# Performance work log

Hardware: AMD Instinct MI355X
Metric: run time of the kernel (lower is better)

## Reference

```python
import jax, jax.numpy as jnp
import numpy as np

N = 50000      # nodes
E = 800000     # edges (avg degree 16)
D = 128        # in_dim
H = 128        # hidden_dim
C = 10         # num_classes
G = 128        # graphs in batch
NUM_LAYERS = 3


def setup_inputs() -> dict:
    key = jax.random.key(0)
    ks = jax.random.split(key, 32)
    inp = {
        'features': jax.random.normal(ks[0], (N, D), dtype=jnp.float32),
        'src': jax.random.randint(ks[1], (E,), 0, N, dtype=jnp.int32),
        'dst': jax.random.randint(ks[2], (E,), 0, N, dtype=jnp.int32),
        'graph_ids': jnp.sort(jax.random.randint(ks[3], (N,), 0, G, dtype=jnp.int32)),
        'eps': jnp.zeros((NUM_LAYERS,), dtype=jnp.float32),  # learn_eps=True, init 0
    }
    # GIN MLPs: layer i has linear1 [in,H], linear2 [H,H] (stored as [in,out])
    ki = 4
    for i in range(NUM_LAYERS):
        din = D if i == 0 else H
        inp[f'w1_{i}'] = jax.random.normal(ks[ki], (din, H), dtype=jnp.float32) * (1.0 / np.sqrt(din)); ki += 1
        inp[f'b1_{i}'] = jnp.zeros((H,), dtype=jnp.float32)
        inp[f'w2_{i}'] = jax.random.normal(ks[ki], (H, H), dtype=jnp.float32) * (1.0 / np.sqrt(H)); ki += 1
        inp[f'b2_{i}'] = jnp.zeros((H,), dtype=jnp.float32)
    inp['wc1'] = jax.random.normal(ks[ki], (H, H), dtype=jnp.float32) * (1.0 / np.sqrt(H)); ki += 1
    inp['bc1'] = jnp.zeros((H,), dtype=jnp.float32)
    inp['wc2'] = jax.random.normal(ks[ki], (H, C), dtype=jnp.float32) * (1.0 / np.sqrt(H)); ki += 1
    inp['bc2'] = jnp.zeros((C,), dtype=jnp.float32)
    return inp


def _mlp(x, w1, b1, w2, b2):
    return jax.nn.relu(x @ w1 + b1) @ w2 + b2


def reference(features, src, dst, graph_ids, eps,
              w1_0, b1_0, w2_0, b2_0,
              w1_1, b1_1, w2_1, b2_1,
              w1_2, b1_2, w2_2, b2_2,
              wc1, bc1, wc2, bc2):
    mlps = [(w1_0, b1_0, w2_0, b2_0), (w1_1, b1_1, w2_1, b2_1), (w1_2, b1_2, w2_2, b2_2)]
    h = features
    for i, (w1, b1, w2, b2) in enumerate(mlps):
        # GINConv: aggregate sum of in-neighbor features (gather src, segment-sum into dst)
        agg = jax.ops.segment_sum(h[src], dst, num_segments=N)
        h = (1.0 + eps[i]) * h + agg
        h = _mlp(h, w1, b1, w2, b2)
        h = jax.nn.relu(h)
    # SumPooling: nodes -> graphs
    hg = jax.ops.segment_sum(h, graph_ids, num_segments=G)  # [G, H]
    out = jax.nn.relu(hg @ wc1 + bc1) @ wc2 + bc2            # [G, C]
    return out
```

## Files before the change

### kernel.cpp

```cpp
#include <hip/hip_runtime.h>

#define NN 50000
#define EE 800000
#define HH 128
#define CC 10
#define GG 128
#define NBK 782
#define NCH 98
#define CHUNK 8192

typedef __attribute__((ext_vector_type(8))) short short8;
typedef __attribute__((ext_vector_type(4))) float f32x4;

__device__ __forceinline__ ushort f2b(float f) {
    union { float f; uint u; } x; x.f = f;
    uint u = x.u;
    uint r = (u + 0x7fffu + ((u >> 16) & 1u)) >> 16;
    return (ushort)r;
}
__device__ __forceinline__ float lo2f(uint v) {
    union { uint u; float f; } x; x.u = v << 16; return x.f;
}
__device__ __forceinline__ float hi2f(uint v) {
    union { uint u; float f; } x; x.u = v & 0xffff0000u; return x.f;
}


__global__ __launch_bounds__(256) void prep_kernel(const float* __restrict__ features,
                                                   const float* w0, const float* w1,
                                                   const float* w2, const float* w3,
                                                   const float* w4, const float* w5,
                                                   const int* __restrict__ dst,
                                                   ushort* __restrict__ hb0,
                                                   ushort* __restrict__ wt,
                                                   int* __restrict__ hist) {
    __shared__ int hc[NBK];
    const int b = blockIdx.x, t = threadIdx.x;
    if (b < 6250) {
        int idx = b * 256 + t;
        float4 v = *(const float4*)(features + (size_t)idx * 4);
        ushort4 o;
        o.x = f2b(v.x); o.y = f2b(v.y); o.z = f2b(v.z); o.w = f2b(v.w);
        *(ushort4*)(hb0 + (size_t)idx * 4) = o;
    } else if (b < 6634) {
        int idx = (b - 6250) * 256 + t;
        int mi = idx >> 14, rest = idx & 16383;
        int n = rest >> 7, k = rest & 127;
        const float* src;
        switch (mi) {
            case 0: src = w0; break; case 1: src = w1; break;
            case 2: src = w2; break; case 3: src = w3; break;
            case 4: src = w4; break; default: src = w5; break;
        }
        wt[mi * 16384 + n * 128 + k] = f2b(src[k * 128 + n]);
    } else {
        const int c = b - 6634;
        for (int k = t; k < NBK; k += 256) hc[k] = 0;
        __syncthreads();
        for (int j = 0; j < 32; ++j) {
            int e = c * CHUNK + j * 256 + t;
            if (e < EE) atomicAdd(&hc[dst[e] >> 6], 1);
        }
        __syncthreads();
        for (int k = t; k < NBK; k += 256) hist[k * NCH + c] = hc[k];
    }
}

__global__ __launch_bounds__(128) void bscan_kernel(const int* __restrict__ hist,
                                                    int* __restrict__ rel,
                                                    int* __restrict__ btot) {
    __shared__ int s[128];
    const int b = blockIdx.x, t = threadIdx.x;
    int v = (t < NCH) ? hist[b * NCH + t] : 0;
    s[t] = v;
    __syncthreads();
    for (int off = 1; off < 128; off <<= 1) {
        int tt = (t >= off) ? s[t - off] : 0;
        __syncthreads();
        s[t] += tt;
        __syncthreads();
    }
    if (t < NCH) rel[b * NCH + t] = s[t] - v;
    if (t == 127) btot[b] = s[127];
}

__global__ __launch_bounds__(1024) void tscan_kernel(const int* __restrict__ btot,
                                                     int* __restrict__ bucketptr,
                                                     int* __restrict__ rowptr) {
    __shared__ int s[1024];
    const int t = threadIdx.x;
    int v = (t < NBK) ? btot[t] : 0;
    s[t] = v;
    __syncthreads();
    for (int off = 1; off < 1024; off <<= 1) {
        int tt = (t >= off) ? s[t - off] : 0;
        __syncthreads();
        s[t] += tt;
        __syncthreads();
    }
    if (t < NBK) bucketptr[t] = s[t] - v;
    if (t == 0) { bucketptr[NBK] = EE; rowptr[NN] = EE; }
}

__global__ __launch_bounds__(256) void scatter_kernel(const int* __restrict__ src,
                                                      const int* __restrict__ dst,
                                                      const int* __restrict__ rel,
                                                      const int* __restrict__ bucketptr,
                                                      int* __restrict__ epk) {
    __shared__ int cur[NBK];
    const int c = blockIdx.x, t = threadIdx.x;
    for (int k = t; k < NBK; k += 256) cur[k] = bucketptr[k] + rel[k * NCH + c];
    __syncthreads();
    for (int j = 0; j < 32; ++j) {
        int e = c * CHUNK + j * 256 + t;
        if (e < EE) {
            int d = dst[e];
            int bk = d >> 6;
            int pos = atomicAdd(&cur[bk], 1);
            epk[pos] = ((d & 63) << 16) | src[e];
        }
    }
}

__global__ __launch_bounds__(256) void bsort_kernel(const int* __restrict__ epk,
                                                    const int* __restrict__ bucketptr,
                                                    ushort* __restrict__ eidx,
                                                    int* __restrict__ rowptr) {
    __shared__ int cnt[64];
    __shared__ int cur[64];
    const int b = blockIdx.x, t = threadIdx.x;
    const int base = bucketptr[b], end = bucketptr[b + 1];
    if (t < 64) cnt[t] = 0;
    __syncthreads();
    for (int i = base + t; i < end; i += 256)
        atomicAdd(&cnt[(epk[i] >> 16) & 63], 1);
    __syncthreads();
    if (t < 64) {
        int v = cnt[t];
        int incl = v;
#pragma unroll
        for (int off = 1; off < 64; off <<= 1) {
            int u = __shfl_up(incl, off);
            if (t >= off) incl += u;
        }
        int excl = incl - v;
        cur[t] = excl;
        int node = b * 64 + t;
        if (node < NN) rowptr[node] = base + excl;
    }
    __syncthreads();
    for (int i = base + t; i < end; i += 256) {
        int p = epk[i];
        int dl = (p >> 16) & 63;
        int pos = atomicAdd(&cur[dl], 1);
        eidx[base + pos] = (ushort)(p & 0xffff);
    }
}


__global__ __launch_bounds__(256) void aggregate_kernel(const ushort* __restrict__ h,
                                                        const int* __restrict__ rowptr,
                                                        const ushort* __restrict__ eidx,
                                                        const float* __restrict__ epsp,
                                                        int layer,
                                                        ushort* __restrict__ xb) {
    const int node = blockIdx.x * 8 + (threadIdx.x >> 5);
    if (node >= NN) return;
    const int li = threadIdx.x & 31;
    const int beg = rowptr[node], end = rowptr[node + 1];
    float c0 = 0.f, c1 = 0.f, c2 = 0.f, c3 = 0.f;
    int i = beg;
    for (; i + 8 <= end; i += 8) {
        int s[8];
        uint2 v[8];
#pragma unroll
        for (int k = 0; k < 8; ++k) s[k] = eidx[i + k];
#pragma unroll
        for (int k = 0; k < 8; ++k)
            v[k] = *(const uint2*)(h + (size_t)s[k] * HH + li * 4);
#pragma unroll
        for (int k = 0; k < 8; ++k) {
            c0 += lo2f(v[k].x); c1 += hi2f(v[k].x);
            c2 += lo2f(v[k].y); c3 += hi2f(v[k].y);
        }
    }
    for (; i < end; ++i) {
        int s = eidx[i];
        uint2 v = *(const uint2*)(h + (size_t)s * HH + li * 4);
        c0 += lo2f(v.x); c1 += hi2f(v.x);
        c2 += lo2f(v.y); c3 += hi2f(v.y);
    }
    uint2 hv = *(const uint2*)(h + (size_t)node * HH + li * 4);
    const float e = 1.0f + epsp[layer];
    ushort4 o;
    o.x = f2b(e * lo2f(hv.x) + c0);
    o.y = f2b(e * hi2f(hv.x) + c1);
    o.z = f2b(e * lo2f(hv.y) + c2);
    o.w = f2b(e * hi2f(hv.y) + c3);
    *(ushort4*)(xb + (size_t)node * HH + li * 4) = o;
}


template <bool LAST>
__global__ __launch_bounds__(256) void fused_mlp(const ushort* __restrict__ xb,
                                                 const ushort* __restrict__ wt1,
                                                 const ushort* __restrict__ wt2,
                                                 const float* __restrict__ b1,
                                                 const float* __restrict__ b2,
                                                 const int* __restrict__ gid,
                                                 float* __restrict__ hg,
                                                 ushort* __restrict__ out, int nrows) {
    __shared__ __align__(16) ushort xs[64][136];
    __shared__ __align__(16) ushort hs[64][136];
    const int tid = threadIdx.x;
    const int lane = tid & 63, w = tid >> 6;
    const int row0 = blockIdx.x * 64;
    const int l15 = lane & 15, lhi = lane >> 4;

    short8 a1[2][4], a2[2][4];
#pragma unroll
    for (int fa = 0; fa < 2; ++fa)
#pragma unroll
        for (int kt = 0; kt < 4; ++kt) {
            int n = w * 32 + fa * 16 + l15;
            int k = kt * 32 + lhi * 8;
            a1[fa][kt] = *(const short8*)(wt1 + n * HH + k);
            a2[fa][kt] = *(const short8*)(wt2 + n * HH + k);
        }

#pragma unroll
    for (int it = 0; it < 4; ++it) {
        int idx = it * 256 + tid;
        int r = idx >> 4, kq = idx & 15;
        int row = row0 + r;
        uint4 xv = make_uint4(0u, 0u, 0u, 0u);
        if (row < nrows) xv = *(const uint4*)(xb + (size_t)row * HH + kq * 8);
        *(uint4*)&xs[r][kq * 8] = xv;
    }
    __syncthreads();

    f32x4 acc[2][4];
#pragma unroll
    for (int fa = 0; fa < 2; ++fa)
#pragma unroll
        for (int fb = 0; fb < 4; ++fb) acc[fa][fb] = (f32x4)(0.f);
#pragma unroll
    for (int kt = 0; kt < 4; ++kt) {
        short8 bfr[4];
#pragma unroll
        for (int fb = 0; fb < 4; ++fb)
            bfr[fb] = *(const short8*)&xs[fb * 16 + l15][kt * 32 + lhi * 8];
#pragma unroll
        for (int fa = 0; fa < 2; ++fa)
#pragma unroll
            for (int fb = 0; fb < 4; ++fb)
                acc[fa][fb] = __builtin_amdgcn_mfma_f32_16x16x32_bf16(a1[fa][kt], bfr[fb],
                                                                     acc[fa][fb], 0, 0, 0);
    }

#pragma unroll
    for (int fa = 0; fa < 2; ++fa) {
        int nb = w * 32 + fa * 16 + lhi * 4;
        float4 bv = *(const float4*)(b1 + nb);
#pragma unroll
        for (int fb = 0; fb < 4; ++fb) {
            ushort4 o;
            o.x = f2b(fmaxf(acc[fa][fb][0] + bv.x, 0.f));
            o.y = f2b(fmaxf(acc[fa][fb][1] + bv.y, 0.f));
            o.z = f2b(fmaxf(acc[fa][fb][2] + bv.z, 0.f));
            o.w = f2b(fmaxf(acc[fa][fb][3] + bv.w, 0.f));
            *(ushort4*)&hs[fb * 16 + l15][nb] = o;
        }
    }
    __syncthreads();

#pragma unroll
    for (int fa = 0; fa < 2; ++fa)
#pragma unroll
        for (int fb = 0; fb < 4; ++fb) acc[fa][fb] = (f32x4)(0.f);
#pragma unroll
    for (int kt = 0; kt < 4; ++kt) {
        short8 bfr[4];
#pragma unroll
        for (int fb = 0; fb < 4; ++fb)
            bfr[fb] = *(const short8*)&hs[fb * 16 + l15][kt * 32 + lhi * 8];
#pragma unroll
        for (int fa = 0; fa < 2; ++fa)
#pragma unroll
            for (int fb = 0; fb < 4; ++fb)
                acc[fa][fb] = __builtin_amdgcn_mfma_f32_16x16x32_bf16(a2[fa][kt], bfr[fb],
                                                                     acc[fa][fb], 0, 0, 0);
    }

#pragma unroll
    for (int fa = 0; fa < 2; ++fa) {
        int nb = w * 32 + fa * 16 + lhi * 4;
        float4 bv = *(const float4*)(b2 + nb);
#pragma unroll
        for (int fb = 0; fb < 4; ++fb) {
            int m = row0 + fb * 16 + l15;
            ushort4 o;
            o.x = f2b(fmaxf(acc[fa][fb][0] + bv.x, 0.f));
            o.y = f2b(fmaxf(acc[fa][fb][1] + bv.y, 0.f));
            o.z = f2b(fmaxf(acc[fa][fb][2] + bv.z, 0.f));
            o.w = f2b(fmaxf(acc[fa][fb][3] + bv.w, 0.f));
            if (LAST) {
                *(ushort4*)&xs[fb * 16 + l15][nb] = o;
            } else if (m < nrows) {
                *(ushort4*)(out + (size_t)m * HH + nb) = o;
            }
        }
    }

    if (LAST) {
        __syncthreads();
        int j = tid & 63;
        int rg = tid >> 6;
        float ax = 0.f, ay = 0.f;
        int gcur = -1;
#pragma unroll
        for (int ii = 0; ii < 16; ++ii) {
            int r = rg + ii * 4;
            int n = row0 + r;
            if (n >= nrows) break;
            int g = gid[n];
            if (g != gcur) {
                if (gcur >= 0) {
                    atomicAdd(&hg[gcur * HH + 2 * j], ax);
                    atomicAdd(&hg[gcur * HH + 2 * j + 1], ay);
                }
                gcur = g; ax = 0.f; ay = 0.f;
            }
            uint v = *(const uint*)&xs[r][2 * j];
            ax += lo2f(v); ay += hi2f(v);
        }
        if (gcur >= 0) {
            atomicAdd(&hg[gcur * HH + 2 * j], ax);
            atomicAdd(&hg[gcur * HH + 2 * j + 1], ay);
        }
    }
}


__global__ __launch_bounds__(128) void classify_kernel(const float* __restrict__ hg,
                                                       const float* __restrict__ wc1,
                                                       const float* __restrict__ bc1,
                                                       const float* __restrict__ wc2,
                                                       const float* __restrict__ bc2,
                                                       float* __restrict__ out) {
    __shared__ float xrow[HH];
    __shared__ float trow[HH];
    int g = blockIdx.x, j = threadIdx.x;
    xrow[j] = hg[g * HH + j];
    __syncthreads();
    float s = bc1[j];
#pragma unroll 8
    for (int k = 0; k < HH; ++k) s += xrow[k] * wc1[k * HH + j];
    trow[j] = fmaxf(s, 0.f);
    __syncthreads();
    if (j < CC) {
        float o = bc2[j];
#pragma unroll 8
        for (int k = 0; k < HH; ++k) o += trow[k] * wc2[k * CC + j];
        out[g * CC + j] = o;
    }
}

extern "C" void kernel_launch(void* const* d_in, const int* in_sizes, int n_in,
                              void* d_out, int out_size, void* d_ws, size_t ws_size,
                              hipStream_t stream) {
    const float* features = (const float*)d_in[0];
    const int* src = (const int*)d_in[1];
    const int* dst = (const int*)d_in[2];
    const int* gid = (const int*)d_in[3];
    const float* eps = (const float*)d_in[4];
    const float* w1[3] = {(const float*)d_in[5], (const float*)d_in[9], (const float*)d_in[13]};
    const float* b1[3] = {(const float*)d_in[6], (const float*)d_in[10], (const float*)d_in[14]};
    const float* w2[3] = {(const float*)d_in[7], (const float*)d_in[11], (const float*)d_in[15]};
    const float* b2[3] = {(const float*)d_in[8], (const float*)d_in[12], (const float*)d_in[16]};
    const float* wc1 = (const float*)d_in[17];
    const float* bc1 = (const float*)d_in[18];
    const float* wc2 = (const float*)d_in[19];
    const float* bc2 = (const float*)d_in[20];
    float* outp = (float*)d_out;

    char* ws = (char*)d_ws;
    size_t off = 0;
    auto alloc = [&](size_t bytes) {
        void* p = ws + off;
        off += (bytes + 255) & ~(size_t)255;
        return p;
    };
    int* hist = (int*)alloc((size_t)NBK * NCH * sizeof(int));
    int* rel = (int*)alloc((size_t)NBK * NCH * sizeof(int));
    int* btot = (int*)alloc(NBK * sizeof(int));
    int* bucketptr = (int*)alloc((NBK + 1) * sizeof(int));
    int* epk = (int*)alloc(EE * sizeof(int));
    ushort* eidx = (ushort*)alloc(EE * sizeof(ushort));
    int* rowptr = (int*)alloc((NN + 1) * sizeof(int));
    ushort* hb0 = (ushort*)alloc((size_t)NN * HH * 2);
    ushort* hbuf = (ushort*)alloc((size_t)NN * HH * 2);
    ushort* xb = (ushort*)alloc((size_t)NN * HH * 2);
    ushort* wtb = (ushort*)alloc(6 * 16384 * 2);
    float* hg = (float*)alloc(GG * HH * sizeof(float));

    prep_kernel<<<6732, 256, 0, stream>>>(features, w1[0], w2[0], w1[1], w2[1], w1[2], w2[2],
                                          dst, hb0, wtb, hist);
    bscan_kernel<<<NBK, 128, 0, stream>>>(hist, rel, btot);
    tscan_kernel<<<1, 1024, 0, stream>>>(btot, bucketptr, rowptr);
    scatter_kernel<<<NCH, 256, 0, stream>>>(src, dst, rel, bucketptr, epk);
    bsort_kernel<<<NBK, 256, 0, stream>>>(epk, bucketptr, eidx, rowptr);

    hipMemsetAsync(hg, 0, GG * HH * sizeof(float), stream);

    const int GB = (NN + 63) / 64;
    const int AB = (NN + 7) / 8;

    aggregate_kernel<<<AB, 256, 0, stream>>>(hb0, rowptr, eidx, eps, 0, xb);
    fused_mlp<false><<<GB, 256, 0, stream>>>(xb, wtb + 0 * 16384, wtb + 1 * 16384,
                                             b1[0], b2[0], gid, hg, hbuf, NN);
    aggregate_kernel<<<AB, 256, 0, stream>>>(hbuf, rowptr, eidx, eps, 1, xb);
    fused_mlp<false><<<GB, 256, 0, stream>>>(xb, wtb + 2 * 16384, wtb + 3 * 16384,
                                             b1[1], b2[1], gid, hg, hbuf, NN);
    aggregate_kernel<<<AB, 256, 0, stream>>>(hbuf, rowptr, eidx, eps, 2, xb);
    fused_mlp<true><<<GB, 256, 0, stream>>>(xb, wtb + 4 * 16384, wtb + 5 * 16384,
                                            b1[2], b2[2], gid, hg, nullptr, NN);

    classify_kernel<<<GG, 128, 0, stream>>>(hg, wc1, bc1, wc2, bc2, outp);
}
```

Measured before the change: 230.2 us.

## Process two row tiles per MLP block with prefetch, fold memset, batch aggregate tail

The fused MLP now handles 128 rows per block as two 64-row tiles. The second tile's global loads are issued before the first tile's compute and written to shared memory afterwards, so the load latency overlaps with MFMA work and the weight-fragment loads are amortized over twice as many rows. The zeroing of hg moves into extra blocks of the prep kernel, which removes the separate memset launch. The aggregate kernel's remainder loop becomes one batched 8-wide gather with clamped indices and predicated accumulation, exposing more memory-level parallelism at the cost of redundant loads. Halving the number of MLP blocks and doubling shared memory per block can reduce occupancy.

```diff
diff --git a/kernel.cpp b/kernel.cpp
--- a/kernel.cpp
+++ b/kernel.cpp
@@ -33,7 +33,8 @@
                                                    const int* __restrict__ dst,
                                                    ushort* __restrict__ hb0,
                                                    ushort* __restrict__ wt,
-                                                   int* __restrict__ hist) {
+                                                   int* __restrict__ hist,
+                                                   float* __restrict__ hg) {
     __shared__ int hc[NBK];
     const int b = blockIdx.x, t = threadIdx.x;
     if (b < 6250) {
@@ -53,7 +54,7 @@
             case 4: src = w4; break; default: src = w5; break;
         }
         wt[mi * 16384 + n * 128 + k] = f2b(src[k * 128 + n]);
-    } else {
+    } else if (b < 6732) {
         const int c = b - 6634;
         for (int k = t; k < NBK; k += 256) hc[k] = 0;
         __syncthreads();
@@ -63,6 +64,9 @@
         }
         __syncthreads();
         for (int k = t; k < NBK; k += 256) hist[k * NCH + c] = hc[k];
+    } else {
+        int idx = (b - 6732) * 256 + t;
+        hg[idx] = 0.f;
     }
 }
 
@@ -184,11 +188,24 @@
             c2 += lo2f(v[k].y); c3 += hi2f(v[k].y);
         }
     }
-    for (; i < end; ++i) {
-        int s = eidx[i];
-        uint2 v = *(const uint2*)(h + (size_t)s * HH + li * 4);
-        c0 += lo2f(v.x); c1 += hi2f(v.x);
-        c2 += lo2f(v.y); c3 += hi2f(v.y);
+    if (i < end) {
+        int s[8];
+        uint2 v[8];
+#pragma unroll
+        for (int k = 0; k < 8; ++k) {
+            int idx = i + k;
+            s[k] = eidx[idx < end ? idx : end - 1];
+        }
+#pragma unroll
+        for (int k = 0; k < 8; ++k)
+            v[k] = *(const uint2*)(h + (size_t)s[k] * HH + li * 4);
+#pragma unroll
+        for (int k = 0; k < 8; ++k) {
+            if (i + k < end) {
+                c0 += lo2f(v[k].x); c1 += hi2f(v[k].x);
+                c2 += lo2f(v[k].y); c3 += hi2f(v[k].y);
+            }
+        }
     }
     uint2 hv = *(const uint2*)(h + (size_t)node * HH + li * 4);
     const float e = 1.0f + epsp[layer];
@@ -210,12 +227,22 @@
                                                  const int* __restrict__ gid,
                                                  float* __restrict__ hg,
                                                  ushort* __restrict__ out, int nrows) {
-    __shared__ __align__(16) ushort xs[64][136];
+    __shared__ __align__(16) ushort xs[2][64][136];
     __shared__ __align__(16) ushort hs[64][136];
     const int tid = threadIdx.x;
     const int lane = tid & 63, w = tid >> 6;
-    const int row0 = blockIdx.x * 64;
+    const int row0 = blockIdx.x * 128;
     const int l15 = lane & 15, lhi = lane >> 4;
+    const int sr = tid >> 4, skq = tid & 15;
+
+    uint4 st[4];
+#pragma unroll
+    for (int it = 0; it < 4; ++it) {
+        int r = it * 16 + sr;
+        int row = row0 + r;
+        st[it] = make_uint4(0u, 0u, 0u, 0u);
+        if (row < nrows) st[it] = *(const uint4*)(xb + (size_t)row * HH + skq * 8);
+    }
 
     short8 a1[2][4], a2[2][4];
 #pragma unroll
@@ -229,114 +256,119 @@
         }
 
 #pragma unroll
+    for (int it = 0; it < 4; ++it) *(uint4*)&xs[0][it * 16 + sr][skq * 8] = st[it];
+    __syncthreads();
+
+#pragma unroll
     for (int it = 0; it < 4; ++it) {
-        int idx = it * 256 + tid;
-        int r = idx >> 4, kq = idx & 15;
-        int row = row0 + r;
-        uint4 xv = make_uint4(0u, 0u, 0u, 0u);
-        if (row < nrows) xv = *(const uint4*)(xb + (size_t)row * HH + kq * 8);
-        *(uint4*)&xs[r][kq * 8] = xv;
-    }
-    __syncthreads();
+        int r = it * 16 + sr;
+        int row = row0 + 64 + r;
+        st[it] = make_uint4(0u, 0u, 0u, 0u);
+        if (row < nrows) st[it] = *(const uint4*)(xb + (size_t)row * HH + skq * 8);
+    }
 
     f32x4 acc[2][4];
 #pragma unroll
-    for (int fa = 0; fa < 2; ++fa)
-#pragma unroll
-        for (int fb = 0; fb < 4; ++fb) acc[fa][fb] = (f32x4)(0.f);
-#pragma unroll
-    for (int kt = 0; kt < 4; ++kt) {
-        short8 bfr[4];
-#pragma unroll
-        for (int fb = 0; fb < 4; ++fb)
-            bfr[fb] = *(const short8*)&xs[fb * 16 + l15][kt * 32 + lhi * 8];
+    for (int tile = 0; tile < 2; ++tile) {
+        const int rt0 = row0 + tile * 64;
 #pragma unroll
         for (int fa = 0; fa < 2; ++fa)
 #pragma unroll
+            for (int fb = 0; fb < 4; ++fb) acc[fa][fb] = (f32x4)(0.f);
+#pragma unroll
+        for (int kt = 0; kt < 4; ++kt) {
+            short8 bfr[4];
+#pragma unroll
             for (int fb = 0; fb < 4; ++fb)
-                acc[fa][fb] = __builtin_amdgcn_mfma_f32_16x16x32_bf16(a1[fa][kt], bfr[fb],
-                                                                     acc[fa][fb], 0, 0, 0);
-    }
-
-#pragma unroll
-    for (int fa = 0; fa < 2; ++fa) {
-        int nb = w * 32 + fa * 16 + lhi * 4;
-        float4 bv = *(const float4*)(b1 + nb);
-#pragma unroll
-        for (int fb = 0; fb < 4; ++fb) {
-            ushort4 o;
-            o.x = f2b(fmaxf(acc[fa][fb][0] + bv.x, 0.f));
-            o.y = f2b(fmaxf(acc[fa][fb][1] + bv.y, 0.f));
-            o.z = f2b(fmaxf(acc[fa][fb][2] + bv.z, 0.f));
-            o.w = f2b(fmaxf(acc[fa][fb][3] + bv.w, 0.f));
-            *(ushort4*)&hs[fb * 16 + l15][nb] = o;
-        }
-    }
-    __syncthreads();
-
-#pragma unroll
-    for (int fa = 0; fa < 2; ++fa)
-#pragma unroll
-        for (int fb = 0; fb < 4; ++fb) acc[fa][fb] = (f32x4)(0.f);
-#pragma unroll
-    for (int kt = 0; kt < 4; ++kt) {
-        short8 bfr[4];
-#pragma unroll
-        for (int fb = 0; fb < 4; ++fb)
-            bfr[fb] = *(const short8*)&hs[fb * 16 + l15][kt * 32 + lhi * 8];
+                bfr[fb] = *(const short8*)&xs[tile][fb * 16 + l15][kt * 32 + lhi * 8];
+#pragma unroll
+            for (int fa = 0; fa < 2; ++fa)
+#pragma unroll
+                for (int fb = 0; fb < 4; ++fb)
+                    acc[fa][fb] = __builtin_amdgcn_mfma_f32_16x16x32_bf16(a1[fa][kt], bfr[fb],
+                                                                         acc[fa][fb], 0, 0, 0);
+        }
+#pragma unroll
+        for (int fa = 0; fa < 2; ++fa) {
+            int nb = w * 32 + fa * 16 + lhi * 4;
+            float4 bv = *(const float4*)(b1 + nb);
+#pragma unroll
+            for (int fb = 0; fb < 4; ++fb) {
+                ushort4 o;
+                o.x = f2b(fmaxf(acc[fa][fb][0] + bv.x, 0.f));
+                o.y = f2b(fmaxf(acc[fa][fb][1] + bv.y, 0.f));
+                o.z = f2b(fmaxf(acc[fa][fb][2] + bv.z, 0.f));
+                o.w = f2b(fmaxf(acc[fa][fb][3] + bv.w, 0.f));
+                *(ushort4*)&hs[fb * 16 + l15][nb] = o;
+            }
+        }
+        __syncthreads();
 #pragma unroll
         for (int fa = 0; fa < 2; ++fa)
 #pragma unroll
+            for (int fb = 0; fb < 4; ++fb) acc[fa][fb] = (f32x4)(0.f);
+#pragma unroll
+        for (int kt = 0; kt < 4; ++kt) {
+            short8 bfr[4];
+#pragma unroll
             for (int fb = 0; fb < 4; ++fb)
-                acc[fa][fb] = __builtin_amdgcn_mfma_f32_16x16x32_bf16(a2[fa][kt], bfr[fb],
-                                                                     acc[fa][fb], 0, 0, 0);
-    }
-
-#pragma unroll
-    for (int fa = 0; fa < 2; ++fa) {
-        int nb = w * 32 + fa * 16 + lhi * 4;
-        float4 bv = *(const float4*)(b2 + nb);
-#pragma unroll
-        for (int fb = 0; fb < 4; ++fb) {
-            int m = row0 + fb * 16 + l15;
-            ushort4 o;
-            o.x = f2b(fmaxf(acc[fa][fb][0] + bv.x, 0.f));
-            o.y = f2b(fmaxf(acc[fa][fb][1] + bv.y, 0.f));
-            o.z = f2b(fmaxf(acc[fa][fb][2] + bv.z, 0.f));
-            o.w = f2b(fmaxf(acc[fa][fb][3] + bv.w, 0.f));
-            if (LAST) {
-                *(ushort4*)&xs[fb * 16 + l15][nb] = o;
-            } else if (m < nrows) {
-                *(ushort4*)(out + (size_t)m * HH + nb) = o;
+                bfr[fb] = *(const short8*)&hs[fb * 16 + l15][kt * 32 + lhi * 8];
+#pragma unroll
+            for (int fa = 0; fa < 2; ++fa)
+#pragma unroll
+                for (int fb = 0; fb < 4; ++fb)
+                    acc[fa][fb] = __builtin_amdgcn_mfma_f32_16x16x32_bf16(a2[fa][kt], bfr[fb],
+                                                                         acc[fa][fb], 0, 0, 0);
+        }
+#pragma unroll
+        for (int fa = 0; fa < 2; ++fa) {
+            int nb = w * 32 + fa * 16 + lhi * 4;
+            float4 bv = *(const float4*)(b2 + nb);
+#pragma unroll
+            for (int fb = 0; fb < 4; ++fb) {
+                int m = rt0 + fb * 16 + l15;
+                ushort4 o;
+                o.x = f2b(fmaxf(acc[fa][fb][0] + bv.x, 0.f));
+                o.y = f2b(fmaxf(acc[fa][fb][1] + bv.y, 0.f));
+                o.z = f2b(fmaxf(acc[fa][fb][2] + bv.z, 0.f));
+                o.w = f2b(fmaxf(acc[fa][fb][3] + bv.w, 0.f));
+                if (LAST) {
+                    *(ushort4*)&xs[tile][fb * 16 + l15][nb] = o;
+                } else if (m < nrows) {
+                    *(ushort4*)(out + (size_t)m * HH + nb) = o;
+                }
             }
         }
-    }
-
-    if (LAST) {
-        __syncthreads();
-        int j = tid & 63;
-        int rg = tid >> 6;
-        float ax = 0.f, ay = 0.f;
-        int gcur = -1;
-#pragma unroll
-        for (int ii = 0; ii < 16; ++ii) {
-            int r = rg + ii * 4;
-            int n = row0 + r;
-            if (n >= nrows) break;
-            int g = gid[n];
-            if (g != gcur) {
-                if (gcur >= 0) {
-                    atomicAdd(&hg[gcur * HH + 2 * j], ax);
-                    atomicAdd(&hg[gcur * HH + 2 * j + 1], ay);
+        if (tile == 0) {
+#pragma unroll
+            for (int it = 0; it < 4; ++it) *(uint4*)&xs[1][it * 16 + sr][skq * 8] = st[it];
+        }
+        __syncthreads();
+        if (LAST) {
+            int j = tid & 63;
+            int rg = tid >> 6;
+            float ax = 0.f, ay = 0.f;
+            int gcur = -1;
+#pragma unroll
+            for (int ii = 0; ii < 16; ++ii) {
+                int r = rg + ii * 4;
+                int n = rt0 + r;
+                if (n >= nrows) break;
+                int g = gid[n];
+                if (g != gcur) {
+                    if (gcur >= 0) {
+                        atomicAdd(&hg[gcur * HH + 2 * j], ax);
+                        atomicAdd(&hg[gcur * HH + 2 * j + 1], ay);
+                    }
+                    gcur = g; ax = 0.f; ay = 0.f;
                 }
-                gcur = g; ax = 0.f; ay = 0.f;
+                uint v = *(const uint*)&xs[tile][r][2 * j];
+                ax += lo2f(v); ay += hi2f(v);
             }
-            uint v = *(const uint*)&xs[r][2 * j];
-            ax += lo2f(v); ay += hi2f(v);
-        }
-        if (gcur >= 0) {
-            atomicAdd(&hg[gcur * HH + 2 * j], ax);
-            atomicAdd(&hg[gcur * HH + 2 * j + 1], ay);
+            if (gcur >= 0) {
+                atomicAdd(&hg[gcur * HH + 2 * j], ax);
+                atomicAdd(&hg[gcur * HH + 2 * j + 1], ay);
+            }
         }
     }
 }
@@ -404,16 +436,14 @@
     ushort* wtb = (ushort*)alloc(6 * 16384 * 2);
     float* hg = (float*)alloc(GG * HH * sizeof(float));
 
-    prep_kernel<<<6732, 256, 0, stream>>>(features, w1[0], w2[0], w1[1], w2[1], w1[2], w2[2],
-                                          dst, hb0, wtb, hist);
+    prep_kernel<<<6796, 256, 0, stream>>>(features, w1[0], w2[0], w1[1], w2[1], w1[2], w2[2],
+                                          dst, hb0, wtb, hist, hg);
     bscan_kernel<<<NBK, 128, 0, stream>>>(hist, rel, btot);
     tscan_kernel<<<1, 1024, 0, stream>>>(btot, bucketptr, rowptr);
     scatter_kernel<<<NCH, 256, 0, stream>>>(src, dst, rel, bucketptr, epk);
     bsort_kernel<<<NBK, 256, 0, stream>>>(epk, bucketptr, eidx, rowptr);
 
-    hipMemsetAsync(hg, 0, GG * HH * sizeof(float), stream);
-
-    const int GB = (NN + 63) / 64;
+    const int GB = (NN + 127) / 128;
     const int AB = (NN + 7) / 8;
 
     aggregate_kernel<<<AB, 256, 0, stream>>>(hb0, rowptr, eidx, eps, 0, xb);
```

New measurement: 206.9 us. -10.1%, faster.
